# Kernel optimization log

Hardware: AMD Instinct MI355X
Metric: run time of the kernel (lower is better)

## Reference

```python
import jax, jax.numpy as jnp
import numpy as np

B = 2048
DIMS = [300, 74, 35]
R = 3
ENC = 150
HID = 32
CAT = ENC * R  # 450


def setup_inputs() -> dict:
    key = jax.random.key(0)
    ks = jax.random.split(key, 32)
    d = {}
    for i, dim in enumerate(DIMS):
        d[f"x{i}"] = jax.random.normal(ks[i], (B, 1, dim), dtype=jnp.float32)
    s = 0.05
    for i, dim in enumerate(DIMS):
        d[f"encW{i}"] = jax.random.normal(ks[3 + 2 * i], (ENC, dim), dtype=jnp.float32) * s
        d[f"encb{i}"] = jax.random.normal(ks[4 + 2 * i], (ENC,), dtype=jnp.float32) * s
    d["affw"] = jax.random.normal(ks[10], (R,), dtype=jnp.float32) * s      # Linear(1,1) weight per branch
    d["Ww"] = jax.random.normal(ks[11], (R, HID, 1), dtype=jnp.float32) * s  # Linear(1,32)
    d["Wc"] = jax.random.normal(ks[12], (R, HID, CAT), dtype=jnp.float32) * s  # Linear(450,32)
    d["Wh"] = jax.random.normal(ks[13], (R, 1, HID), dtype=jnp.float32) * s   # Linear(32,1)
    d["clsW1"] = jax.random.normal(ks[14], (128, CAT), dtype=jnp.float32) * s
    d["clsb1"] = jax.random.normal(ks[15], (128,), dtype=jnp.float32) * s
    d["clsW2"] = jax.random.normal(ks[16], (7, 128), dtype=jnp.float32) * s
    d["clsb2"] = jax.random.normal(ks[17], (7,), dtype=jnp.float32) * s
    return d


def reference(x0, x1, x2, encW0, encb0, encW1, encb1, encW2, encb2,
              affw, Ww, Wc, Wh, clsW1, clsb1, clsW2, clsb2):
    xs = [x0, x1, x2]
    encW = [encW0, encW1, encW2]
    encb = [encb0, encb1, encb2]
    # Encode each modality: [B,1,dim_i] -> [B,1,150]
    enc = [jnp.einsum('btd,ed->bte', xs[i], encW[i]) + encb[i] for i in range(R)]
    feat_n = jnp.concatenate(enc, axis=2)            # [B,1,450]
    scale = 1.0 / jnp.sqrt(jnp.float32(feat_n.shape[1]))  # T=1
    att_feats = []
    for i in range(R):
        enc_t = jnp.swapaxes(enc[i], 1, 2)           # [B,150,1]
        t = jnp.swapaxes(feat_n, 1, 2) * affw[i]     # [B,450,1] (Linear(1,1), no bias)
        # outer product attention: [B,150,1] @ [B,1,450] -> [B,150,450]
        att = jnp.tanh(jnp.matmul(enc_t, jnp.swapaxes(t, 1, 2)) * scale)
        a = jnp.einsum('bec,hc->beh', att, Wc[i])    # [B,150,32]
        b = jnp.matmul(enc_t, Ww[i].T)               # [B,150,1]@[1,32] -> [B,150,32]
        H = jax.nn.relu(a + b)
        out_i = jnp.swapaxes(jnp.matmul(H, Wh[i].T), 1, 2) + enc[i]  # [B,1,150]
        att_feats.append(out_i)
    feats = jnp.concatenate(att_feats, axis=2)       # [B,1,450]
    # classifier (dropout is identity in eval mode)
    h = jnp.einsum('btc,kc->btk', feats, clsW1) + clsb1
    return jnp.einsum('btk,ok->bto', h, clsW2) + clsb2
```

## Files before the change

kernel.cpp:

```cpp
#include <hip/hip_runtime.h>
#include <math.h>

#define NJ 9
#define DEG 17
#define X0f 3.0f

struct Poly { float c[NJ]; };

#define FMA4(A,S,W) do { (A).x = fmaf((S),(W).x,(A).x); (A).y = fmaf((S),(W).y,(A).y); \
                         (A).z = fmaf((S),(W).z,(A).z); (A).w = fmaf((S),(W).w,(A).w); } while(0)

__global__ __launch_bounds__(256) void k_repack(
    const float* __restrict__ Wc, const float* __restrict__ W1,
    const float* __restrict__ eW0, const float* __restrict__ eW1, const float* __restrict__ eW2,
    float* __restrict__ WcT, float* __restrict__ W1T,
    float* __restrict__ Wt0, float* __restrict__ Wt1, float* __restrict__ Wt2) {
    int tid = blockIdx.x * 256 + threadIdx.x;
    int stride = gridDim.x * 256;
    for (int idx = tid; idx < 3 * 464 * 32; idx += stride) {
        int i = idx / (464 * 32); int rem = idx - i * 464 * 32;
        int m = rem >> 5, h = rem & 31;
        float v = 0.f;
        if (m < 456) {
            int seg = m / 152, e = m - seg * 152;
            if (e < 150) v = Wc[((size_t)i * 32 + h) * 450 + seg * 150 + e];
        }
        WcT[idx] = v;
    }
    for (int idx = tid; idx < 456 * 128; idx += stride) {
        int m = idx >> 7, k = idx & 127;
        int seg = m / 152, e = m - seg * 152;
        W1T[idx] = (e < 150) ? W1[k * 450 + seg * 150 + e] : 0.f;
    }
    for (int idx = tid; idx < 304 * 152; idx += stride) {
        int d = idx / 152, e = idx - d * 152;
        Wt0[idx] = (d < 300 && e < 150) ? eW0[e * 300 + d] : 0.f;
    }
    for (int idx = tid; idx < 76 * 152; idx += stride) {
        int d = idx / 152, e = idx - d * 152;
        Wt1[idx] = (d < 74 && e < 150) ? eW1[e * 74 + d] : 0.f;
    }
    for (int idx = tid; idx < 36 * 152; idx += stride) {
        int d = idx / 152, e = idx - d * 152;
        Wt2[idx] = (d < 35 && e < 150) ? eW2[e * 35 + d] : 0.f;
    }
}

__global__ __launch_bounds__(768, 1) void k_fused(
    const float* __restrict__ x0, const float* __restrict__ x1, const float* __restrict__ x2,
    const float* __restrict__ eb0, const float* __restrict__ eb1, const float* __restrict__ eb2,
    const float* __restrict__ Wt0, const float* __restrict__ Wt1, const float* __restrict__ Wt2,
    const float* __restrict__ WcT,
    const float* __restrict__ affw, const float* __restrict__ Ww, const float* __restrict__ Wh,
    const float* __restrict__ W1T, const float* __restrict__ cb1,
    const float* __restrict__ cW2, const float* __restrict__ cb2,
    float* __restrict__ out, Poly pc) {
    __shared__ __align__(16) float xs[8][428];
    __shared__ __align__(16) float feat[8][468];
    __shared__ __align__(16) float fo[8][468];
    __shared__ unsigned smaxu[8];

    int tid = threadIdx.x;
    int b0 = blockIdx.x * 8;

    if (tid < 8) smaxu[tid] = 0u;
    if (tid < 64) feat[tid >> 3][456 + (tid & 7)] = 0.f;
    for (int idx = tid; idx < 8 * 304; idx += 768) {
        int b = idx / 304, d = idx - b * 304;
        xs[b][d] = (d < 300) ? x0[(size_t)(b0 + b) * 300 + d] : 0.f;
    }
    for (int idx = tid; idx < 8 * 76; idx += 768) {
        int b = idx / 76, d = idx - b * 76;
        xs[b][304 + d] = (d < 74) ? x1[(size_t)(b0 + b) * 74 + d] : 0.f;
    }
    for (int idx = tid; idx < 8 * 36; idx += 768) {
        int b = idx / 36, d = idx - b * 36;
        xs[b][380 + d] = (d < 35) ? x2[(size_t)(b0 + b) * 35 + d] : 0.f;
    }
    __syncthreads();

    {
        int tasks[2]; int nt = 1;
        tasks[0] = tid;
        if (tid >= 624) { tasks[nt++] = 768 + (767 - tid); }
        for (int q = 0; q < nt; ++q) {
            int task = tasks[q];
            int b = task & 7, m4 = task >> 3;
            int seg = (m4 >= 76) ? 2 : (m4 >= 38) ? 1 : 0;
            int e4 = m4 - seg * 38;
            const float* eb = seg == 0 ? eb0 : seg == 1 ? eb1 : eb2;
            const float4* Wt4 = (const float4*)(seg == 0 ? Wt0 : seg == 1 ? Wt1 : Wt2) + e4;
            const float4* xr = (const float4*)&xs[b][seg == 0 ? 0 : seg == 1 ? 304 : 380];
            int DP4 = seg == 0 ? 76 : seg == 1 ? 19 : 9;
            int e = e4 * 4;
            float4 acc;
            acc.x = (e     < 150) ? eb[e]     : 0.f;
            acc.y = (e + 1 < 150) ? eb[e + 1] : 0.f;
            acc.z = (e + 2 < 150) ? eb[e + 2] : 0.f;
            acc.w = (e + 3 < 150) ? eb[e + 3] : 0.f;
            for (int d4 = 0; d4 < DP4; ++d4) {
                float4 x4 = xr[d4];
                float4 w0 = Wt4[(d4 * 4 + 0) * 38];
                float4 w1 = Wt4[(d4 * 4 + 1) * 38];
                float4 w2 = Wt4[(d4 * 4 + 2) * 38];
                float4 w3 = Wt4[(d4 * 4 + 3) * 38];
                FMA4(acc, x4.x, w0);
                FMA4(acc, x4.y, w1);
                FMA4(acc, x4.z, w2);
                FMA4(acc, x4.w, w3);
            }
            ((float4*)&feat[b][0])[m4] = acc;
            float mx = fmaxf(fmaxf(fabsf(acc.x), fabsf(acc.y)), fmaxf(fabsf(acc.z), fabsf(acc.w)));
            atomicMax(&smaxu[b], __float_as_uint(mx));
        }
    }
    __syncthreads();

    {
        int w = tid >> 6;
        int i = w >> 2;
        int wp = w & 3;
        int lane = tid & 63;
        int hq = lane & 7, slice = (lane >> 3) & 3, bh = lane >> 5;
        int b = wp * 2 + bh;
        float aff = affw[i];
        const float4* Wb4 = (const float4*)WcT + (size_t)i * 464 * 8 + hq;
        const float4* frow = (const float4*)&feat[b][0];

        float4 acc[NJ];
        #pragma unroll
        for (int J = 0; J < NJ; ++J) acc[J] = make_float4(0.f, 0.f, 0.f, 0.f);

        int m4lo = slice * 29, m4hi = m4lo + 29;
        for (int m4 = m4lo; m4 < m4hi; ++m4) {
            float4 f4 = frow[m4];
            #pragma unroll
            for (int r = 0; r < 4; ++r) {
                float fv = (r == 0) ? f4.x : (r == 1) ? f4.y : (r == 2) ? f4.z : f4.w;
                float g = aff * fv;
                float g2 = g * g;
                float4 wv = Wb4[(m4 * 4 + r) * 8];
                float p = g;
                FMA4(acc[0], p, wv);
                #pragma unroll
                for (int J = 1; J < NJ; ++J) { p *= g2; FMA4(acc[J], p, wv); }
            }
        }
        #pragma unroll
        for (int J = 0; J < NJ; ++J) {
            float cJ = pc.c[J];
            float vx = acc[J].x; vx += __shfl_xor(vx, 8); vx += __shfl_xor(vx, 16);
            float vy = acc[J].y; vy += __shfl_xor(vy, 8); vy += __shfl_xor(vy, 16);
            float vz = acc[J].z; vz += __shfl_xor(vz, 8); vz += __shfl_xor(vz, 16);
            float vw = acc[J].w; vw += __shfl_xor(vw, 8); vw += __shfl_xor(vw, 16);
            acc[J].x = vx * cJ; acc[J].y = vy * cJ; acc[J].z = vz * cJ; acc[J].w = vw * cJ;
        }

        float4 wW4 = ((const float4*)(Ww + i * 32))[hq];
        float4 wH4 = ((const float4*)(Wh + i * 32))[hq];
        float gmax = fabsf(aff) * __uint_as_float(smaxu[b]);
        int e4lo = slice * 10;
        int e4hi = (slice == 3) ? 38 : (e4lo + 10);
        for (int e4 = e4lo; e4 < e4hi; ++e4) {
            float4 s4 = frow[i * 38 + e4];
            float ores[4];
            #pragma unroll
            for (int r = 0; r < 4; ++r) {
                float s = (r == 0) ? s4.x : (r == 1) ? s4.y : (r == 2) ? s4.z : s4.w;
                float4 a4;
                if (fabsf(s) * gmax <= X0f) {
                    float s2 = s * s, p = s;
                    a4.x = acc[0].x * p; a4.y = acc[0].y * p;
                    a4.z = acc[0].z * p; a4.w = acc[0].w * p;
                    #pragma unroll
                    for (int J = 1; J < NJ; ++J) { p *= s2; FMA4(a4, p, acc[J]); }
                } else {
                    a4 = make_float4(0.f, 0.f, 0.f, 0.f);
                    for (int c = 0; c < 456; ++c) {
                        float t = tanhf(s * aff * feat[b][c]);
                        float4 wv = Wb4[c * 8];
                        FMA4(a4, t, wv);
                    }
                }
                float hx = fmaxf(fmaf(s, wW4.x, a4.x), 0.f);
                float hy = fmaxf(fmaf(s, wW4.y, a4.y), 0.f);
                float hz = fmaxf(fmaf(s, wW4.z, a4.z), 0.f);
                float hw = fmaxf(fmaf(s, wW4.w, a4.w), 0.f);
                float csum = hx * wH4.x + hy * wH4.y + hz * wH4.z + hw * wH4.w;
                csum += __shfl_xor(csum, 1);
                csum += __shfl_xor(csum, 2);
                csum += __shfl_xor(csum, 4);
                ores[r] = csum + s;
            }
            if (hq == 0)
                ((float4*)&fo[b][0])[i * 38 + e4] = make_float4(ores[0], ores[1], ores[2], ores[3]);
        }
    }
    __syncthreads();

    {
        int cs = tid >> 8;
        int rr = tid & 255;
        int b = rr >> 5, k4 = rr & 31;
        const float4* W14 = (const float4*)W1T + k4;
        const float4* fr = (const float4*)&fo[b][0];
        float4 a = make_float4(0.f, 0.f, 0.f, 0.f);
        int c4lo = cs * 38, c4hi = c4lo + 38;
        for (int c4 = c4lo; c4 < c4hi; ++c4) {
            float4 fv = fr[c4];
            float4 w0 = W14[(c4 * 4 + 0) * 32];
            float4 w1 = W14[(c4 * 4 + 1) * 32];
            float4 w2 = W14[(c4 * 4 + 2) * 32];
            float4 w3 = W14[(c4 * 4 + 3) * 32];
            FMA4(a, fv.x, w0);
            FMA4(a, fv.y, w1);
            FMA4(a, fv.z, w2);
            FMA4(a, fv.w, w3);
        }
        ((float4*)&xs[0][0])[(cs * 8 + b) * 33 + k4] = a;
    }
    __syncthreads();
    if (tid < 256) {
        int b = tid >> 5, k4 = tid & 31;
        const float4* hp4 = (const float4*)&xs[0][0];
        float4 a = hp4[(b) * 33 + k4];
        float4 p1 = hp4[(8 + b) * 33 + k4];
        float4 p2 = hp4[(16 + b) * 33 + k4];
        float4 bias = ((const float4*)cb1)[k4];
        a.x += p1.x + p2.x + bias.x;
        a.y += p1.y + p2.y + bias.y;
        a.z += p1.z + p2.z + bias.z;
        a.w += p1.w + p2.w + bias.w;
        ((float4*)&feat[b][0])[k4] = a;
    }
    __syncthreads();
    if (tid < 56) {
        int b = tid / 7, o = tid - (tid / 7) * 7;
        const float4* h4 = (const float4*)&feat[b][0];
        const float4* w4 = (const float4*)(cW2 + o * 128);
        float4 a4 = make_float4(0.f, 0.f, 0.f, 0.f);
        #pragma unroll 8
        for (int k4 = 0; k4 < 32; ++k4) {
            float4 h = h4[k4], w = w4[k4];
            a4.x = fmaf(h.x, w.x, a4.x); a4.y = fmaf(h.y, w.y, a4.y);
            a4.z = fmaf(h.z, w.z, a4.z); a4.w = fmaf(h.w, w.w, a4.w);
        }
        out[(size_t)(b0 + b) * 7 + o] = cb2[o] + a4.x + a4.y + a4.z + a4.w;
    }
}

static void make_poly(float* cf) {
    const double a = 3.0;
    const int NQ = 128;
    const double PI = 3.14159265358979323846;
    double b[DEG + 1];
    for (int k = 0; k <= DEG; ++k) b[k] = 0.0;
    for (int m = 0; m < NQ; ++m) {
        double th = PI * (m + 0.5) / NQ;
        double f = tanh(a * cos(th));
        for (int k = 1; k <= DEG; k += 2)
            b[k] += (2.0 / NQ) * f * cos(k * th);
    }
    double Tp[DEG + 1], Tc[DEG + 1], Tn[DEG + 1], mono[DEG + 1];
    for (int j = 0; j <= DEG; ++j) { Tp[j] = 0; Tc[j] = 0; mono[j] = 0; }
    Tp[0] = 1.0;
    Tc[1] = 1.0;
    for (int j = 0; j <= DEG; ++j) mono[j] += b[1] * Tc[j];
    for (int k = 2; k <= DEG; ++k) {
        for (int j = 0; j <= DEG; ++j) Tn[j] = -Tp[j];
        for (int j = 1; j <= DEG; ++j) Tn[j] += 2.0 * Tc[j - 1];
        for (int j = 0; j <= DEG; ++j) { Tp[j] = Tc[j]; Tc[j] = Tn[j]; }
        if (k & 1) for (int j = 0; j <= DEG; ++j) mono[j] += b[k] * Tc[j];
    }
    for (int J = 0; J < NJ; ++J) {
        int j = 2 * J + 1;
        cf[J] = (float)(mono[j] / pow(a, (double)j));
    }
}

extern "C" void kernel_launch(void* const* d_in, const int* in_sizes, int n_in,
                              void* d_out, int out_size, void* d_ws, size_t ws_size,
                              hipStream_t stream) {
    (void)in_sizes; (void)n_in; (void)out_size; (void)ws_size;
    const float* x0    = (const float*)d_in[0];
    const float* x1    = (const float*)d_in[1];
    const float* x2    = (const float*)d_in[2];
    const float* eW0   = (const float*)d_in[3];
    const float* eb0   = (const float*)d_in[4];
    const float* eW1   = (const float*)d_in[5];
    const float* eb1   = (const float*)d_in[6];
    const float* eW2   = (const float*)d_in[7];
    const float* eb2   = (const float*)d_in[8];
    const float* affw  = (const float*)d_in[9];
    const float* Ww    = (const float*)d_in[10];
    const float* Wc    = (const float*)d_in[11];
    const float* Wh    = (const float*)d_in[12];
    const float* cW1   = (const float*)d_in[13];
    const float* cb1   = (const float*)d_in[14];
    const float* cW2   = (const float*)d_in[15];
    const float* cb2   = (const float*)d_in[16];

    float* ws    = (float*)d_ws;
    float* wsWcT = ws;
    float* wsW1T = ws + 44544;
    float* wsWt0 = ws + 102912;
    float* wsWt1 = ws + 149120;
    float* wsWt2 = ws + 160672;

    Poly pc;
    make_poly(pc.c);

    k_repack<<<dim3(96), dim3(256), 0, stream>>>(Wc, cW1, eW0, eW1, eW2,
                                                 wsWcT, wsW1T, wsWt0, wsWt1, wsWt2);
    k_fused<<<dim3(256), dim3(768), 0, stream>>>(x0, x1, x2, eb0, eb1, eb2,
                                                 wsWt0, wsWt1, wsWt2, wsWcT,
                                                 affw, Ww, Wh, wsW1T, cb1, cW2, cb2,
                                                 (float*)d_out, pc);
}
```

Baseline: 77.11 us.

## Restructure fused kernel work split with atomics and lower polynomial degree

Rewrites every stage of the fused kernel. The encoder now splits segment 0 into two halves accumulated with shared-memory atomicAdd, and reads x1/x2 directly from global memory. The attention moment accumulation is split across polynomial-order halves and column halves, reduced through LDS atomics into a shared moment buffer, and the per-element evaluation maps one lane per feature element. The tanh polynomial degree is lowered from 17 to 15, and the classifier split is reorganized. The aim is more balanced work and fewer register-heavy shuffles, at the cost of more shared-memory atomics, an extra barrier, and reduced polynomial accuracy.

After: 119.8 us. +55.3%, slower.

```diff
diff --git a/kernel.cpp b/kernel.cpp
--- a/kernel.cpp
+++ b/kernel.cpp
@@ -1,8 +1,8 @@
 #include <hip/hip_runtime.h>
 #include <math.h>
 
-#define NJ 9
-#define DEG 17
+#define NJ 8
+#define DEG 15
 #define X0f 3.0f
 
 struct Poly { float c[NJ]; };
@@ -55,197 +55,201 @@
     const float* __restrict__ W1T, const float* __restrict__ cb1,
     const float* __restrict__ cW2, const float* __restrict__ cb2,
     float* __restrict__ out, Poly pc) {
-    __shared__ __align__(16) float xs[8][428];
-    __shared__ __align__(16) float feat[8][468];
-    __shared__ __align__(16) float fo[8][468];
+    __shared__ __align__(16) float R[6912];
+    __shared__ __align__(16) float featf[8 * 468];
+    __shared__ __align__(16) float fof[8 * 468];
+    __shared__ __align__(16) float wWs[96], wHs[96];
     __shared__ unsigned smaxu[8];
 
     int tid = threadIdx.x;
     int b0 = blockIdx.x * 8;
 
+    for (int k = tid; k < 8 * 468; k += 768) featf[k] = 0.f;
     if (tid < 8) smaxu[tid] = 0u;
-    if (tid < 64) feat[tid >> 3][456 + (tid & 7)] = 0.f;
-    for (int idx = tid; idx < 8 * 304; idx += 768) {
-        int b = idx / 304, d = idx - b * 304;
-        xs[b][d] = (d < 300) ? x0[(size_t)(b0 + b) * 300 + d] : 0.f;
-    }
-    for (int idx = tid; idx < 8 * 76; idx += 768) {
-        int b = idx / 76, d = idx - b * 76;
-        xs[b][304 + d] = (d < 74) ? x1[(size_t)(b0 + b) * 74 + d] : 0.f;
-    }
-    for (int idx = tid; idx < 8 * 36; idx += 768) {
-        int b = idx / 36, d = idx - b * 36;
-        xs[b][380 + d] = (d < 35) ? x2[(size_t)(b0 + b) * 35 + d] : 0.f;
+    if (tid < 96) { wWs[tid] = Ww[tid]; wHs[tid] = Wh[tid]; }
+    if (tid >= 96 && tid < 144) {
+        int q = tid - 96; int b = q / 6, r = q - b * 6;
+        fof[b * 468 + (r >> 1) * 152 + 150 + (r & 1)] = 0.f;
+    }
+    for (int idx = tid; idx < 600; idx += 768) {
+        int b = idx / 75, q = idx - b * 75;
+        ((float4*)(R + b * 304))[q] = ((const float4*)(x0 + (size_t)(b0 + b) * 300))[q];
     }
     __syncthreads();
 
     {
-        int tasks[2]; int nt = 1;
-        tasks[0] = tid;
-        if (tid >= 624) { tasks[nt++] = 768 + (767 - tid); }
-        for (int q = 0; q < nt; ++q) {
-            int task = tasks[q];
-            int b = task & 7, m4 = task >> 3;
-            int seg = (m4 >= 76) ? 2 : (m4 >= 38) ? 1 : 0;
-            int e4 = m4 - seg * 38;
+        int w = tid >> 6, lane = tid & 63, g = lane >> 3, b = lane & 7;
+        for (int s = w * 8 + g; s < 152; s += 96) {
+            int seg, e4, dlo, dhi, addBias;
+            if (s < 76)       { seg = 0; e4 = s >> 1; dlo = (s & 1) * 152; dhi = (s & 1) ? 300 : 152; addBias = !(s & 1); }
+            else if (s < 114) { seg = 1; e4 = s - 76;  dlo = 0; dhi = 74; addBias = 1; }
+            else              { seg = 2; e4 = s - 114; dlo = 0; dhi = 35; addBias = 1; }
             const float* eb = seg == 0 ? eb0 : seg == 1 ? eb1 : eb2;
-            const float4* Wt4 = (const float4*)(seg == 0 ? Wt0 : seg == 1 ? Wt1 : Wt2) + e4;
-            const float4* xr = (const float4*)&xs[b][seg == 0 ? 0 : seg == 1 ? 304 : 380];
-            int DP4 = seg == 0 ? 76 : seg == 1 ? 19 : 9;
+            const float4* W4 = (const float4*)(seg == 0 ? Wt0 : seg == 1 ? Wt1 : Wt2) + e4;
             int e = e4 * 4;
-            float4 acc;
-            acc.x = (e     < 150) ? eb[e]     : 0.f;
-            acc.y = (e + 1 < 150) ? eb[e + 1] : 0.f;
-            acc.z = (e + 2 < 150) ? eb[e + 2] : 0.f;
-            acc.w = (e + 3 < 150) ? eb[e + 3] : 0.f;
-            for (int d4 = 0; d4 < DP4; ++d4) {
-                float4 x4 = xr[d4];
-                float4 w0 = Wt4[(d4 * 4 + 0) * 38];
-                float4 w1 = Wt4[(d4 * 4 + 1) * 38];
-                float4 w2 = Wt4[(d4 * 4 + 2) * 38];
-                float4 w3 = Wt4[(d4 * 4 + 3) * 38];
-                FMA4(acc, x4.x, w0);
-                FMA4(acc, x4.y, w1);
-                FMA4(acc, x4.z, w2);
-                FMA4(acc, x4.w, w3);
+            float4 acc = make_float4(0.f, 0.f, 0.f, 0.f);
+            if (addBias) {
+                acc.x = (e     < 150) ? eb[e]     : 0.f;
+                acc.y = (e + 1 < 150) ? eb[e + 1] : 0.f;
+                acc.z = (e + 2 < 150) ? eb[e + 2] : 0.f;
+                acc.w = (e + 3 < 150) ? eb[e + 3] : 0.f;
             }
-            ((float4*)&feat[b][0])[m4] = acc;
-            float mx = fmaxf(fmaxf(fabsf(acc.x), fabsf(acc.y)), fmaxf(fabsf(acc.z), fabsf(acc.w)));
-            atomicMax(&smaxu[b], __float_as_uint(mx));
-        }
-    }
+            if (seg == 0) {
+                const float* xb = R + b * 304;
+                #pragma unroll 4
+                for (int d = dlo; d < dhi; ++d) { float xv = xb[d]; float4 wv = W4[d * 38]; FMA4(acc, xv, wv); }
+            } else if (seg == 1) {
+                const float* xb = x1 + (size_t)(b0 + b) * 74;
+                #pragma unroll 2
+                for (int d = 0; d < 74; ++d) { float xv = xb[d]; float4 wv = W4[d * 38]; FMA4(acc, xv, wv); }
+            } else {
+                const float* xb = x2 + (size_t)(b0 + b) * 35;
+                #pragma unroll 5
+                for (int d = 0; d < 35; ++d) { float xv = xb[d]; float4 wv = W4[d * 38]; FMA4(acc, xv, wv); }
+            }
+            float* dst = featf + b * 468 + seg * 152 + e;
+            atomicAdd(dst + 0, acc.x); atomicAdd(dst + 1, acc.y);
+            atomicAdd(dst + 2, acc.z); atomicAdd(dst + 3, acc.w);
+        }
+    }
+    __syncthreads();
+
+    for (int k = tid; k < 6912; k += 768) R[k] = 0.f;
     __syncthreads();
 
     {
         int w = tid >> 6;
-        int i = w >> 2;
-        int wp = w & 3;
-        int lane = tid & 63;
-        int hq = lane & 7, slice = (lane >> 3) & 3, bh = lane >> 5;
-        int b = wp * 2 + bh;
+        int i = w >> 2, jh = (w >> 1) & 1, cs = w & 1;
+        int lane = tid & 63, hq = lane & 7, b = lane >> 3;
         float aff = affw[i];
-        const float4* Wb4 = (const float4*)WcT + (size_t)i * 464 * 8 + hq;
-        const float4* frow = (const float4*)&feat[b][0];
-
-        float4 acc[NJ];
+        const float4* Wb4 = (const float4*)WcT + (size_t)i * 3712 + hq;
+        const float* fb = featf + b * 468;
+        float4 acc[4];
+        acc[0] = acc[1] = acc[2] = acc[3] = make_float4(0.f, 0.f, 0.f, 0.f);
+        float mx = 0.f;
+        int clo = cs * 228;
+        #pragma unroll 2
+        for (int c = clo; c < clo + 228; ++c) {
+            float fv = fb[c];
+            float4 wv = Wb4[(size_t)c * 8];
+            mx = fmaxf(mx, fabsf(fv));
+            float g = aff * fv, g2 = g * g;
+            float p0;
+            if (jh == 0) p0 = g;
+            else { float g4 = g2 * g2; p0 = g4 * g4 * g; }
+            float p1 = p0 * g2, p2 = p1 * g2, p3 = p2 * g2;
+            FMA4(acc[0], p0, wv); FMA4(acc[1], p1, wv);
+            FMA4(acc[2], p2, wv); FMA4(acc[3], p3, wv);
+        }
+        float* Mb = R + ((i * 8 + jh * 4) * 8 + b) * 36 + hq * 4;
         #pragma unroll
-        for (int J = 0; J < NJ; ++J) acc[J] = make_float4(0.f, 0.f, 0.f, 0.f);
-
-        int m4lo = slice * 29, m4hi = m4lo + 29;
-        for (int m4 = m4lo; m4 < m4hi; ++m4) {
-            float4 f4 = frow[m4];
-            #pragma unroll
-            for (int r = 0; r < 4; ++r) {
-                float fv = (r == 0) ? f4.x : (r == 1) ? f4.y : (r == 2) ? f4.z : f4.w;
-                float g = aff * fv;
-                float g2 = g * g;
-                float4 wv = Wb4[(m4 * 4 + r) * 8];
-                float p = g;
-                FMA4(acc[0], p, wv);
-                #pragma unroll
-                for (int J = 1; J < NJ; ++J) { p *= g2; FMA4(acc[J], p, wv); }
-            }
-        }
+        for (int r = 0; r < 4; ++r) {
+            float cJ = pc.c[jh * 4 + r];
+            float* p = Mb + r * 288;
+            atomicAdd(p + 0, acc[r].x * cJ); atomicAdd(p + 1, acc[r].y * cJ);
+            atomicAdd(p + 2, acc[r].z * cJ); atomicAdd(p + 3, acc[r].w * cJ);
+        }
+        if (i == 0 && jh == 0 && hq == 0) atomicMax(&smaxu[b], __float_as_uint(mx));
+    }
+    __syncthreads();
+
+    {
+        int w = tid >> 6, lane = tid & 63;
         #pragma unroll
-        for (int J = 0; J < NJ; ++J) {
-            float cJ = pc.c[J];
-            float vx = acc[J].x; vx += __shfl_xor(vx, 8); vx += __shfl_xor(vx, 16);
-            float vy = acc[J].y; vy += __shfl_xor(vy, 8); vy += __shfl_xor(vy, 16);
-            float vz = acc[J].z; vz += __shfl_xor(vz, 8); vz += __shfl_xor(vz, 16);
-            float vw = acc[J].w; vw += __shfl_xor(vw, 8); vw += __shfl_xor(vw, 16);
-            acc[J].x = vx * cJ; acc[J].y = vy * cJ; acc[J].z = vz * cJ; acc[J].w = vw * cJ;
-        }
-
-        float4 wW4 = ((const float4*)(Ww + i * 32))[hq];
-        float4 wH4 = ((const float4*)(Wh + i * 32))[hq];
-        float gmax = fabsf(aff) * __uint_as_float(smaxu[b]);
-        int e4lo = slice * 10;
-        int e4hi = (slice == 3) ? 38 : (e4lo + 10);
-        for (int e4 = e4lo; e4 < e4hi; ++e4) {
-            float4 s4 = frow[i * 38 + e4];
-            float ores[4];
-            #pragma unroll
-            for (int r = 0; r < 4; ++r) {
-                float s = (r == 0) ? s4.x : (r == 1) ? s4.y : (r == 2) ? s4.z : s4.w;
-                float4 a4;
+        for (int pp = 0; pp < 2; ++pp) {
+            int pair = w * 2 + pp;
+            int i = pair >> 3, b = pair & 7;
+            float aff = affw[i];
+            float gmax = fabsf(aff) * __uint_as_float(smaxu[b]);
+            const float* fb = featf + b * 468;
+            const float4* M40 = (const float4*)R + (i * 64 + b) * 9;
+            const float4* wW4 = (const float4*)wWs + i * 8;
+            const float4* wH4 = (const float4*)wHs + i * 8;
+            for (int e = lane; e < 150; e += 64) {
+                float s = fb[i * 152 + e];
+                float4 a[8];
                 if (fabsf(s) * gmax <= X0f) {
                     float s2 = s * s, p = s;
-                    a4.x = acc[0].x * p; a4.y = acc[0].y * p;
-                    a4.z = acc[0].z * p; a4.w = acc[0].w * p;
                     #pragma unroll
-                    for (int J = 1; J < NJ; ++J) { p *= s2; FMA4(a4, p, acc[J]); }
+                    for (int h4 = 0; h4 < 8; ++h4) {
+                        float4 m = M40[h4];
+                        a[h4].x = m.x * p; a[h4].y = m.y * p; a[h4].z = m.z * p; a[h4].w = m.w * p;
+                    }
+                    #pragma unroll
+                    for (int J = 1; J < NJ; ++J) {
+                        p *= s2;
+                        const float4* Mj = M40 + J * 72;
+                        #pragma unroll
+                        for (int h4 = 0; h4 < 8; ++h4) FMA4(a[h4], p, Mj[h4]);
+                    }
                 } else {
-                    a4 = make_float4(0.f, 0.f, 0.f, 0.f);
+                    #pragma unroll
+                    for (int h4 = 0; h4 < 8; ++h4) a[h4] = make_float4(0.f, 0.f, 0.f, 0.f);
+                    const float4* Wb4 = (const float4*)WcT + (size_t)i * 3712;
                     for (int c = 0; c < 456; ++c) {
-                        float t = tanhf(s * aff * feat[b][c]);
-                        float4 wv = Wb4[c * 8];
-                        FMA4(a4, t, wv);
+                        float t = tanhf(s * aff * fb[c]);
+                        #pragma unroll
+                        for (int h4 = 0; h4 < 8; ++h4) FMA4(a[h4], t, Wb4[(size_t)c * 8 + h4]);
                     }
                 }
-                float hx = fmaxf(fmaf(s, wW4.x, a4.x), 0.f);
-                float hy = fmaxf(fmaf(s, wW4.y, a4.y), 0.f);
-                float hz = fmaxf(fmaf(s, wW4.z, a4.z), 0.f);
-                float hw = fmaxf(fmaf(s, wW4.w, a4.w), 0.f);
-                float csum = hx * wH4.x + hy * wH4.y + hz * wH4.z + hw * wH4.w;
-                csum += __shfl_xor(csum, 1);
-                csum += __shfl_xor(csum, 2);
-                csum += __shfl_xor(csum, 4);
-                ores[r] = csum + s;
+                float o = 0.f;
+                #pragma unroll
+                for (int h4 = 0; h4 < 8; ++h4) {
+                    float4 ww = wW4[h4], wh = wH4[h4], av = a[h4];
+                    o = fmaf(fmaxf(fmaf(s, ww.x, av.x), 0.f), wh.x, o);
+                    o = fmaf(fmaxf(fmaf(s, ww.y, av.y), 0.f), wh.y, o);
+                    o = fmaf(fmaxf(fmaf(s, ww.z, av.z), 0.f), wh.z, o);
+                    o = fmaf(fmaxf(fmaf(s, ww.w, av.w), 0.f), wh.w, o);
+                }
+                fof[b * 468 + i * 152 + e] = o + s;
             }
-            if (hq == 0)
-                ((float4*)&fo[b][0])[i * 38 + e4] = make_float4(ores[0], ores[1], ores[2], ores[3]);
         }
     }
     __syncthreads();
 
     {
-        int cs = tid >> 8;
-        int rr = tid & 255;
-        int b = rr >> 5, k4 = rr & 31;
-        const float4* W14 = (const float4*)W1T + k4;
-        const float4* fr = (const float4*)&fo[b][0];
-        float4 a = make_float4(0.f, 0.f, 0.f, 0.f);
-        int c4lo = cs * 38, c4hi = c4lo + 38;
-        for (int c4 = c4lo; c4 < c4hi; ++c4) {
-            float4 fv = fr[c4];
-            float4 w0 = W14[(c4 * 4 + 0) * 32];
-            float4 w1 = W14[(c4 * 4 + 1) * 32];
-            float4 w2 = W14[(c4 * 4 + 2) * 32];
-            float4 w3 = W14[(c4 * 4 + 3) * 32];
-            FMA4(a, fv.x, w0);
-            FMA4(a, fv.y, w1);
-            FMA4(a, fv.z, w2);
-            FMA4(a, fv.w, w3);
-        }
-        ((float4*)&xs[0][0])[(cs * 8 + b) * 33 + k4] = a;
+        int w = tid >> 6, lane = tid & 63, u = lane & 7, b = lane >> 3;
+        if (w < 8) {
+            int cs = w & 3, half = w >> 2;
+            float4 acc0 = make_float4(0.f, 0.f, 0.f, 0.f), acc1 = acc0;
+            const float* fb = fof + b * 468;
+            const float4* W14 = (const float4*)W1T + half * 16 + u;
+            int clo = cs * 114;
+            #pragma unroll 2
+            for (int c = clo; c < clo + 114; ++c) {
+                float fv = fb[c];
+                float4 w0 = W14[(size_t)c * 32];
+                float4 w1 = W14[(size_t)c * 32 + 8];
+                FMA4(acc0, fv, w0); FMA4(acc1, fv, w1);
+            }
+            float4* hp = (float4*)R + (cs * 8 + b) * 32 + half * 16 + u;
+            hp[0] = acc0; hp[8] = acc1;
+        }
     }
     __syncthreads();
     if (tid < 256) {
         int b = tid >> 5, k4 = tid & 31;
-        const float4* hp4 = (const float4*)&xs[0][0];
-        float4 a = hp4[(b) * 33 + k4];
-        float4 p1 = hp4[(8 + b) * 33 + k4];
-        float4 p2 = hp4[(16 + b) * 33 + k4];
+        const float4* hp4 = (const float4*)R;
+        float4 v  = hp4[(0 * 8 + b) * 32 + k4];
+        float4 v1 = hp4[(1 * 8 + b) * 32 + k4];
+        float4 v2 = hp4[(2 * 8 + b) * 32 + k4];
+        float4 v3 = hp4[(3 * 8 + b) * 32 + k4];
         float4 bias = ((const float4*)cb1)[k4];
-        a.x += p1.x + p2.x + bias.x;
-        a.y += p1.y + p2.y + bias.y;
-        a.z += p1.z + p2.z + bias.z;
-        a.w += p1.w + p2.w + bias.w;
-        ((float4*)&feat[b][0])[k4] = a;
+        v.x += v1.x + v2.x + v3.x + bias.x;
+        v.y += v1.y + v2.y + v3.y + bias.y;
+        v.z += v1.z + v2.z + v3.z + bias.z;
+        v.w += v1.w + v2.w + v3.w + bias.w;
+        ((float4*)(R + 4096))[b * 33 + k4] = v;
     }
     __syncthreads();
     if (tid < 56) {
         int b = tid / 7, o = tid - (tid / 7) * 7;
-        const float4* h4 = (const float4*)&feat[b][0];
-        const float4* w4 = (const float4*)(cW2 + o * 128);
-        float4 a4 = make_float4(0.f, 0.f, 0.f, 0.f);
-        #pragma unroll 8
-        for (int k4 = 0; k4 < 32; ++k4) {
-            float4 h = h4[k4], w = w4[k4];
-            a4.x = fmaf(h.x, w.x, a4.x); a4.y = fmaf(h.y, w.y, a4.y);
-            a4.z = fmaf(h.z, w.z, a4.z); a4.w = fmaf(h.w, w.w, a4.w);
-        }
-        out[(size_t)(b0 + b) * 7 + o] = cb2[o] + a4.x + a4.y + a4.z + a4.w;
+        const float* hb = R + 4096 + b * 132;
+        const float* w2 = cW2 + o * 128;
+        float acc = cb2[o];
+        #pragma unroll 4
+        for (int k = 0; k < 128; ++k) acc = fmaf(hb[k], w2[k], acc);
+        out[(size_t)(b0 + b) * 7 + o] = acc;
     }
 }
 
```
